# Performance work log

Measured on AMD Instinct MI355X. Metric: run time of the kernel, lower is better.

## Reference

```python
import jax, jax.numpy as jnp
import numpy as np

N_NODES = 100000
N_EDGES = 1000000
D_IN = 64
D_OUT = 64


def setup_inputs() -> dict:
    key = jax.random.key(0)
    k1, k2, k3, k4 = jax.random.split(key, 4)
    x = jax.random.normal(k1, (N_NODES, D_IN), dtype=jnp.float32)
    edge_index = jax.random.randint(k2, (2, N_EDGES), 0, N_NODES, dtype=jnp.int64)
    # Linear layer params (torch Linear convention: W [out, in], b [out])
    W = jax.random.normal(k3, (D_OUT, D_IN), dtype=jnp.float32) * (1.0 / np.sqrt(D_IN))
    b = jax.random.normal(k4, (D_OUT,), dtype=jnp.float32) * 0.01
    return {"x": x, "edge_index": edge_index, "W": W, "b": b}


def reference(x, edge_index, W, b):
    """GCNConv(improved=True) + ReLU.

    improved=True means self-loops with weight 2.0. Instead of concatenating
    self-loop edges, we fold them in analytically: deg += 2 and the self
    contribution is 2 * deg_i^{-1} * x_w[i].
    """
    n = x.shape[0]
    src, dst = edge_index[0], edge_index[1]
    xw = x @ W.T  # [N, D_OUT]
    # degree over destination index, incl. self-loop weight 2.0 (improved)
    deg = jax.ops.segment_sum(jnp.ones_like(src, dtype=xw.dtype), dst,
                              num_segments=n) + jnp.asarray(2.0, xw.dtype)
    dinv = jax.lax.rsqrt(deg)  # no zeros possible (deg >= 2)
    norm = dinv[src] * dinv[dst]  # [E]
    # gather-weight-scatter message passing
    agg = jax.ops.segment_sum(norm[:, None] * xw[src], dst, num_segments=n)
    # self-loop contribution: 2 * dinv_i^2 * xw_i
    agg = agg + (2.0 * dinv * dinv)[:, None] * xw
    return jax.nn.relu(agg + b)
```

## Files before the change

kernel.cpp:

```cpp
#include <hip/hip_runtime.h>
#include <hip/hip_bf16.h>

#define NN 100000
#define NE 1000000
#define D 64
#define BIN_T 4096
#define NB1 245
#define BCAP 768
#define CAP2 96
#define NR 12500
#define NG 125

typedef unsigned int  u32;
typedef unsigned short u16;
typedef __attribute__((ext_vector_type(8))) short bf16x8;
typedef __attribute__((ext_vector_type(4))) float f32x4;

static __device__ __forceinline__ short bfs(float f) {
    union { __hip_bfloat16 h; short s; } u;
    u.h = __float2bfloat16(f);
    return u.s;
}

__global__ __launch_bounds__(256) void bin8_kernel(const int* __restrict__ src,
                                                   const int* __restrict__ dst,
                                                   u32* __restrict__ bins8,
                                                   int* __restrict__ bcnt8) {
    __shared__ int lcur[8];
    const int t = threadIdx.x;
    const int blk = blockIdx.x;
    if (t < 8) lcur[t] = 0;
    __syncthreads();
    const int base = blk * BIN_T;
#pragma unroll
    for (int i = 0; i < 16; ++i) {
        int e = base + i * 256 + t;
        if (e < NE) {
            int d = dst[e];
            int s = src[e];
            int bk = d / NR;
            int pos = atomicAdd(&lcur[bk], 1);
            bins8[(blk * 8 + bk) * BCAP + pos] = (u32)s | ((u32)(d - bk * NR) << 17);
        }
    }
    __syncthreads();
    if (t < 8) bcnt8[blk * 8 + t] = lcur[t];
}

__global__ __launch_bounds__(256) void bin100_kernel(const u32* __restrict__ bins8,
                                                     const int* __restrict__ bcnt8,
                                                     u32* __restrict__ bins100,
                                                     int* __restrict__ cnt100) {
    __shared__ int lcur[100];
    const int bi = blockIdx.x;
    const int r = bi & 7, j = bi >> 3;
    const int t = threadIdx.x;
    const int wid = t >> 6, lane = t & 63;
    if (t < 100) lcur[t] = 0;
    __syncthreads();
    const int f0 = (NB1 * j) >> 5, f1 = (NB1 * (j + 1)) >> 5;
    for (int f = f0 + wid; f < f1; f += 4) {
        const int n = bcnt8[f * 8 + r];
        const u32* p = &bins8[(f * 8 + r) * BCAP];
        for (int i = lane; i < n; i += 64) {
            u32 v = p[i];
            int q = (int)(v >> 17) / NG;
            int pos = atomicAdd(&lcur[q], 1);
            if (pos < CAP2) bins100[(bi * 100 + q) * CAP2 + pos] = v;
        }
    }
    __syncthreads();
    if (t < 100) cnt100[bi * 100 + t] = lcur[t];
}

__global__ __launch_bounds__(256) void build_kernel(const u32* __restrict__ bins100,
                                                    const int* __restrict__ cnt100,
                                                    int* __restrict__ cnt,
                                                    int* __restrict__ esrc) {
    __shared__ int lcnt[NG];
    __shared__ int lslots[NG * 32];
    const int bi = blockIdx.x;
    const int r = bi & 7, q = bi >> 3;
    const int t = threadIdx.x;
    const int wid = t >> 6, lane = t & 63;
    const int nb = r * NR + q * NG;
    if (t < NG) lcnt[t] = 0;
    __syncthreads();
    for (int j = wid; j < 32; j += 4) {
        const int cell = (j * 8 + r) * 100 + q;
        const int n = cnt100[cell];
        const u32* p = &bins100[(size_t)cell * CAP2];
        for (int i = lane; i < n; i += 64) {
            u32 v = p[i];
            int nl = (int)(v >> 17) - q * NG;
            int pos = atomicAdd(&lcnt[nl], 1);
            if (pos < 32) lslots[nl * 32 + pos] = (int)(v & 0x1FFFFu);
        }
    }
    __syncthreads();
    if (t < NG) cnt[nb + t] = lcnt[t];
    for (int i = t; i < NG * 32; i += 256)
        esrc[nb * 32 + i] = lslots[i];
}

__global__ __launch_bounds__(256) void gemm_kernel(const float* __restrict__ x,
                                                   const float* __restrict__ W,
                                                   const int* __restrict__ cnt,
                                                   u16* __restrict__ xs_out) {
    const int t = threadIdx.x;
    if (blockIdx.x == 0 && t < 8)
        *reinterpret_cast<uint4*>(&xs_out[(size_t)NN * D + t * 8]) = make_uint4(0u, 0u, 0u, 0u);

    const int wv  = t >> 6;
    const int l   = t & 63;
    const int job = blockIdx.x * 4 + wv;
    if (job >= NN / 16) return;
    const int r0  = job * 16;
    const int lr  = l & 15;
    const int lg  = l >> 4;

    bf16x8 bfr[4][2];
#pragma unroll
    for (int ct = 0; ct < 4; ++ct) {
#pragma unroll
        for (int h = 0; h < 2; ++h) {
            const float* wp = &W[(ct * 16 + lr) * 64 + h * 32 + lg * 8];
            float4 w0 = *reinterpret_cast<const float4*>(wp);
            float4 w1 = *reinterpret_cast<const float4*>(wp + 4);
            bf16x8 v;
            v[0] = bfs(w0.x); v[1] = bfs(w0.y); v[2] = bfs(w0.z); v[3] = bfs(w0.w);
            v[4] = bfs(w1.x); v[5] = bfs(w1.y); v[6] = bfs(w1.z); v[7] = bfs(w1.w);
            bfr[ct][h] = v;
        }
    }
    bf16x8 afr[2];
#pragma unroll
    for (int h = 0; h < 2; ++h) {
        const float* xp = &x[(size_t)(r0 + lr) * D + h * 32 + lg * 8];
        float4 x0 = *reinterpret_cast<const float4*>(xp);
        float4 x1 = *reinterpret_cast<const float4*>(xp + 4);
        bf16x8 v;
        v[0] = bfs(x0.x); v[1] = bfs(x0.y); v[2] = bfs(x0.z); v[3] = bfs(x0.w);
        v[4] = bfs(x1.x); v[5] = bfs(x1.y); v[6] = bfs(x1.z); v[7] = bfs(x1.w);
        afr[h] = v;
    }

    f32x4 acc[4];
#pragma unroll
    for (int ct = 0; ct < 4; ++ct) acc[ct] = (f32x4){0.f, 0.f, 0.f, 0.f};
#pragma unroll
    for (int ct = 0; ct < 4; ++ct) {
        acc[ct] = __builtin_amdgcn_mfma_f32_16x16x32_bf16(afr[0], bfr[ct][0], acc[ct], 0, 0, 0);
        acc[ct] = __builtin_amdgcn_mfma_f32_16x16x32_bf16(afr[1], bfr[ct][1], acc[ct], 0, 0, 0);
    }

    float dd[4];
#pragma unroll
    for (int j = 0; j < 4; ++j)
        dd[j] = rsqrtf((float)cnt[r0 + lg * 4 + j] + 2.0f);
#pragma unroll
    for (int ct = 0; ct < 4; ++ct)
#pragma unroll
        for (int j = 0; j < 4; ++j)
            xs_out[(size_t)(r0 + lg * 4 + j) * D + ct * 16 + lr] = (u16)bfs(dd[j] * acc[ct][j]);
}

__global__ __launch_bounds__(256) void gather_kernel(const int* __restrict__ cnt,
                                                     const int* __restrict__ esrc,
                                                     const u32* __restrict__ xs,
                                                     const float* __restrict__ b,
                                                     float* __restrict__ out) {
    const int lane = threadIdx.x & 63;
    const int node = (blockIdx.x * 256 + threadIdx.x) >> 6;
    if (node >= NN) return;
    const int mraw = cnt[node];
    const int m    = mraw < 32 ? mraw : 32;
    const int g    = lane >> 3;
    const int c8   = lane & 7;

    int s = esrc[node * 32 + (lane & 31)];

    float a0 = 0, a1 = 0, a2 = 0, a3 = 0, a4 = 0, a5 = 0, a6 = 0, a7 = 0;
    const int iters = (m + 7) >> 3;

#define BODY(kk) {                                                              \
        int idx = (kk) * 8 + g;                                                 \
        int sj = __shfl(s, idx);                                                \
        sj = (idx < m) ? sj : NN;                                               \
        uint4 u = *reinterpret_cast<const uint4*>(&xs[sj * 32 + c8 * 4]);       \
        a0 += __uint_as_float(u.x << 16); a1 += __uint_as_float(u.x & 0xffff0000u); \
        a2 += __uint_as_float(u.y << 16); a3 += __uint_as_float(u.y & 0xffff0000u); \
        a4 += __uint_as_float(u.z << 16); a5 += __uint_as_float(u.z & 0xffff0000u); \
        a6 += __uint_as_float(u.w << 16); a7 += __uint_as_float(u.w & 0xffff0000u); }

    BODY(0) BODY(1)
    for (int k = 2; k < iters; ++k) { BODY(k) }
#undef BODY

#define RED(a) { a += __shfl(a, lane ^ 8); a += __shfl(a, lane ^ 16); a += __shfl(a, lane ^ 32); }
    RED(a0) RED(a1) RED(a2) RED(a3) RED(a4) RED(a5) RED(a6) RED(a7)
#undef RED

    if (g == 0) {
        float dd = rsqrtf((float)mraw + 2.0f);
        uint4 su = *reinterpret_cast<const uint4*>(&xs[node * 32 + c8 * 4]);
        float4 bb0 = *reinterpret_cast<const float4*>(&b[c8 * 8]);
        float4 bb1 = *reinterpret_cast<const float4*>(&b[c8 * 8 + 4]);
        float s0 = __uint_as_float(su.x << 16), s1 = __uint_as_float(su.x & 0xffff0000u);
        float s2 = __uint_as_float(su.y << 16), s3 = __uint_as_float(su.y & 0xffff0000u);
        float s4 = __uint_as_float(su.z << 16), s5 = __uint_as_float(su.z & 0xffff0000u);
        float s6 = __uint_as_float(su.w << 16), s7 = __uint_as_float(su.w & 0xffff0000u);
        float td = 2.0f * dd;
        float4 o0, o1;
        o0.x = fmaxf(fmaf(dd, a0, fmaf(td, s0, bb0.x)), 0.f);
        o0.y = fmaxf(fmaf(dd, a1, fmaf(td, s1, bb0.y)), 0.f);
        o0.z = fmaxf(fmaf(dd, a2, fmaf(td, s2, bb0.z)), 0.f);
        o0.w = fmaxf(fmaf(dd, a3, fmaf(td, s3, bb0.w)), 0.f);
        o1.x = fmaxf(fmaf(dd, a4, fmaf(td, s4, bb1.x)), 0.f);
        o1.y = fmaxf(fmaf(dd, a5, fmaf(td, s5, bb1.y)), 0.f);
        o1.z = fmaxf(fmaf(dd, a6, fmaf(td, s6, bb1.z)), 0.f);
        o1.w = fmaxf(fmaf(dd, a7, fmaf(td, s7, bb1.w)), 0.f);
        *reinterpret_cast<float4*>(&out[node * D + c8 * 8])     = o0;
        *reinterpret_cast<float4*>(&out[node * D + c8 * 8 + 4]) = o1;
    }
}

extern "C" void kernel_launch(void* const* d_in, const int* in_sizes, int n_in,
                              void* d_out, int out_size, void* d_ws, size_t ws_size,
                              hipStream_t stream) {
    const float* x  = (const float*)d_in[0];
    const int*   ei = (const int*)d_in[1];
    const float* W  = (const float*)d_in[2];
    const float* b  = (const float*)d_in[3];
    const int* src = ei;
    const int* dst = ei + NE;
    float* out = (float*)d_out;

    u32* base   = (u32*)d_ws;
    u32* bins8  = base;
    u16* xsb    = (u16*)d_ws;
    u32* bins100= base + 3200032;
    int* cnt100 = (int*)(base + 5657632);
    int* cnt    = (int*)(base + 5683232);
    int* esrc   = (int*)(base + 5783232);
    int* bcnt8  = (int*)(base + 8983232);

    bin8_kernel  <<<NB1, 256, 0, stream>>>(src, dst, bins8, bcnt8);
    bin100_kernel<<<256, 256, 0, stream>>>(bins8, bcnt8, bins100, cnt100);
    build_kernel <<<800, 256, 0, stream>>>(bins100, cnt100, cnt, esrc);
    gemm_kernel  <<<(NN + 63) / 64, 256, 0, stream>>>(x, W, cnt, xsb);
    gather_kernel<<<(NN * 64 + 255) / 256, 256, 0, stream>>>(cnt, esrc, (const u32*)xsb, b, out);
}
```

Measured before the change: 85.33 us.

## Aggregate bin8 atomics per wavefront and flatten build_kernel loop

bin8_kernel now uses ballot/popcount warp aggregation so each wavefront issues a single LDS atomic per bucket, replacing one atomic per edge, and it clamps writes to the bin capacity. build_kernel flattens its per-cell loop into a single strided loop over all slots, with the cell counts preloaded into shared memory, so threads are not left idle on short cells. The gather skips its second unrolled body when a node has eight or fewer neighbours, and the workspace offsets are compacted. The ballot loop adds eight ballots per iteration, which may cost more than the atomics it removes.

New measurement: 109.0 us. +27.7%, slower.

```diff
diff --git a/kernel.cpp b/kernel.cpp
--- a/kernel.cpp
+++ b/kernel.cpp
@@ -12,6 +12,7 @@
 #define NG 125
 
 typedef unsigned int  u32;
+typedef unsigned long long u64;
 typedef unsigned short u16;
 typedef __attribute__((ext_vector_type(8))) short bf16x8;
 typedef __attribute__((ext_vector_type(4))) float f32x4;
@@ -28,19 +29,33 @@
                                                    int* __restrict__ bcnt8) {
     __shared__ int lcur[8];
     const int t = threadIdx.x;
+    const int lane = t & 63;
     const int blk = blockIdx.x;
     if (t < 8) lcur[t] = 0;
     __syncthreads();
     const int base = blk * BIN_T;
-#pragma unroll
+    const u64 below = (lane == 63) ? ~0ull >> 1 : (1ull << lane) - 1ull;
+#pragma unroll 4
     for (int i = 0; i < 16; ++i) {
         int e = base + i * 256 + t;
-        if (e < NE) {
-            int d = dst[e];
-            int s = src[e];
-            int bk = d / NR;
-            int pos = atomicAdd(&lcur[bk], 1);
-            bins8[(blk * 8 + bk) * BCAP + pos] = (u32)s | ((u32)(d - bk * NR) << 17);
+        bool act = e < NE;
+        int d = act ? dst[e] : 0;
+        int s = act ? src[e] : 0;
+        int bk = act ? d / NR : -1;
+        u32 pv = (u32)s | ((u32)(d - bk * NR) << 17);
+#pragma unroll
+        for (int b = 0; b < 8; ++b) {
+            u64 mask = __ballot(bk == b);
+            if (mask == 0ull) continue;
+            int leader = __ffsll((unsigned long long)mask) - 1;
+            int cntb = __popcll(mask);
+            int bs = 0;
+            if (lane == leader) bs = atomicAdd(&lcur[b], cntb);
+            bs = __shfl(bs, leader);
+            if (bk == b) {
+                int pos = bs + __popcll(mask & below);
+                if (pos < BCAP) bins8[(blk * 8 + b) * BCAP + pos] = pv;
+            }
         }
     }
     __syncthreads();
@@ -60,7 +75,8 @@
     __syncthreads();
     const int f0 = (NB1 * j) >> 5, f1 = (NB1 * (j + 1)) >> 5;
     for (int f = f0 + wid; f < f1; f += 4) {
-        const int n = bcnt8[f * 8 + r];
+        int n = bcnt8[f * 8 + r];
+        if (n > BCAP) n = BCAP;
         const u32* p = &bins8[(f * 8 + r) * BCAP];
         for (int i = lane; i < n; i += 64) {
             u32 v = p[i];
@@ -79,25 +95,28 @@
                                                     int* __restrict__ esrc) {
     __shared__ int lcnt[NG];
     __shared__ int lslots[NG * 32];
-    const int bi = blockIdx.x;
-    const int r = bi & 7, q = bi >> 3;
-    const int t = threadIdx.x;
-    const int wid = t >> 6, lane = t & 63;
-    const int nb = r * NR + q * NG;
+    __shared__ int ccnt[32];
+    const int g = blockIdx.x;
+    const int r = g & 7, q = g >> 3;
+    const int t = threadIdx.x;
     if (t < NG) lcnt[t] = 0;
-    __syncthreads();
-    for (int j = wid; j < 32; j += 4) {
-        const int cell = (j * 8 + r) * 100 + q;
-        const int n = cnt100[cell];
-        const u32* p = &bins100[(size_t)cell * CAP2];
-        for (int i = lane; i < n; i += 64) {
-            u32 v = p[i];
+    if (t < 32) {
+        int n = cnt100[((t << 3) | r) * 100 + q];
+        ccnt[t] = n < CAP2 ? n : CAP2;
+    }
+    __syncthreads();
+    for (int i = t; i < 32 * CAP2; i += 256) {
+        int j = i / CAP2;
+        int si = i - j * CAP2;
+        if (si < ccnt[j]) {
+            u32 v = bins100[(size_t)(((j << 3) | r) * 100 + q) * CAP2 + si];
             int nl = (int)(v >> 17) - q * NG;
             int pos = atomicAdd(&lcnt[nl], 1);
             if (pos < 32) lslots[nl * 32 + pos] = (int)(v & 0x1FFFFu);
         }
     }
     __syncthreads();
+    const int nb = r * NR + q * NG;
     if (t < NG) cnt[nb + t] = lcnt[t];
     for (int i = t; i < NG * 32; i += 256)
         esrc[nb * 32 + i] = lslots[i];
@@ -193,7 +212,8 @@
         a4 += __uint_as_float(u.z << 16); a5 += __uint_as_float(u.z & 0xffff0000u); \
         a6 += __uint_as_float(u.w << 16); a7 += __uint_as_float(u.w & 0xffff0000u); }
 
-    BODY(0) BODY(1)
+    BODY(0)
+    if (m > 8) BODY(1)
     for (int k = 2; k < iters; ++k) { BODY(k) }
 #undef BODY
 
@@ -236,14 +256,14 @@
     const int* dst = ei + NE;
     float* out = (float*)d_out;
 
-    u32* base   = (u32*)d_ws;
-    u32* bins8  = base;
-    u16* xsb    = (u16*)d_ws;
-    u32* bins100= base + 3200032;
-    int* cnt100 = (int*)(base + 5657632);
-    int* cnt    = (int*)(base + 5683232);
-    int* esrc   = (int*)(base + 5783232);
-    int* bcnt8  = (int*)(base + 8983232);
+    u32* base    = (u32*)d_ws;
+    u32* bins8   = base;
+    u16* xsb     = (u16*)d_ws;
+    u32* bins100 = base + 1600032;
+    int* cnt100  = (int*)(base + 4057632);
+    int* cnt     = (int*)(base + 4083232);
+    int* esrc    = (int*)(base + 4183232);
+    int* bcnt8   = (int*)(base + 7383232);
 
     bin8_kernel  <<<NB1, 256, 0, stream>>>(src, dst, bins8, bcnt8);
     bin100_kernel<<<256, 256, 0, stream>>>(bins8, bcnt8, bins100, cnt100);
```
